# Performance work log

Hardware: AMD Instinct MI355X
Metric: run time of the kernel (lower is better)

## Reference

```python
import jax, jax.numpy as jnp
import numpy as np
import math

N_HEAD = 16
ROPE_BASE = 10000.0


def _rope_cos_sin(seq_len, head_dim, dtype):
    # standard RoPE tables: freqs_i = base^(-2i/d), i in [0, d/2)
    half = head_dim // 2
    inv_freq = ROPE_BASE ** (-(jnp.arange(half, dtype=jnp.float32) * 2.0 / head_dim))
    t = jnp.arange(seq_len, dtype=jnp.float32)
    ang = t[:, None] * inv_freq[None, :]  # [S, d/2]
    return jnp.cos(ang).astype(dtype), jnp.sin(ang).astype(dtype)


def _apply_rope(x, cos, sin):
    # x: [B, S, H, d]; rotate interleaved even/odd pairs
    x1 = x[..., 0::2]
    x2 = x[..., 1::2]
    c = cos[None, :, None, :]
    s = sin[None, :, None, :]
    out = jnp.stack([x1 * c - x2 * s, x1 * s + x2 * c], axis=-1)
    return out.reshape(x.shape)


def setup_inputs() -> dict:
    key = jax.random.key(0)
    kx, kq, kk, kv, ko = jax.random.split(key, 5)
    B, S, H = 2, 2048, 1024
    x = jax.random.normal(kx, (B, S, H), dtype=jnp.float32)
    scale = 0.02
    w_q = jax.random.normal(kq, (H, H), dtype=jnp.float32) * scale
    w_k = jax.random.normal(kk, (H, H), dtype=jnp.float32) * scale
    w_v = jax.random.normal(kv, (H, H), dtype=jnp.float32) * scale
    w_o = jax.random.normal(ko, (H, H), dtype=jnp.float32) * scale
    return {"x": x, "w_q": w_q, "w_k": w_k, "w_v": w_v, "w_o": w_o}


def reference(x, w_q, w_k, w_v, w_o):
    B, S, H = x.shape
    d = H // N_HEAD
    # torch nn.Linear(bias=False): y = x @ W^T, W is [out, in]
    q = (x @ w_q.T).reshape(B, S, N_HEAD, d)
    k = (x @ w_k.T).reshape(B, S, N_HEAD, d)
    v = (x @ w_v.T).reshape(B, S, N_HEAD, d)
    cos, sin = _rope_cos_sin(S, d, x.dtype)
    q = _apply_rope(q, cos, sin)
    k = _apply_rope(k, cos, sin)
    scores = jnp.einsum("bqhd,bkhd->bhqk", q, k) / math.sqrt(d)
    coefs = jax.nn.softmax(scores, axis=-1)
    # NOTE: causal mask is applied AFTER softmax via tril (no renormalization)
    causal = jnp.tril(jnp.ones((S, S), dtype=bool))
    coefs = jnp.where(causal[None, None], coefs, 0.0)
    out = jnp.einsum("bhqk,bkhd->bqhd", coefs, v).reshape(B, S, H)
    return out @ w_o.T
```

## Files before the change

kernel.cpp:

```cpp
#include <hip/hip_runtime.h>
#include <math.h>

#define SEQ   2048
#define HDIM  1024
#define NH    16
#define DH    64
#define MTOT  4096
#define BHTOT 32

typedef _Float16 half_t;
typedef __attribute__((ext_vector_type(2))) __fp16 fp16x2;
typedef __attribute__((ext_vector_type(4))) _Float16 half4;
typedef __attribute__((ext_vector_type(8))) _Float16 half8;
typedef __attribute__((ext_vector_type(4))) float float4v;

typedef __attribute__((address_space(1))) const unsigned int guint;
typedef __attribute__((address_space(3))) unsigned int luint;
__device__ __forceinline__ void glds16(const half_t* g, half_t* l) {
    __builtin_amdgcn_global_load_lds((guint*)g, (luint*)l, 16, 0, 0);
}

__global__ __launch_bounds__(256)
void prep(const float* __restrict__ x,  const float* __restrict__ wq,
          const float* __restrict__ wk, const float* __restrict__ wv,
          const float* __restrict__ wo,
          half_t* __restrict__ xh,  half_t* __restrict__ wqh,
          half_t* __restrict__ wkh, half_t* __restrict__ wvh,
          half_t* __restrict__ woh, float2* __restrict__ rope)
{
    const int bid = blockIdx.x;
    if (bid < 8192) {
        int i = bid * 256 + threadIdx.x;
        const float* s; half_t* d;
        if (i < 1048576) { s = x; d = xh; }
        else {
            int j = i - 1048576;
            int w = j >> 18; i = j & 262143;
            s = (w == 0) ? wq : (w == 1) ? wk : (w == 2) ? wv : wo;
            d = (w == 0) ? wqh : (w == 1) ? wkh : (w == 2) ? wvh : woh;
        }
        float4 v = ((const float4*)s)[i];
        union { half_t h[4]; uint2 u; } tmp;
        tmp.h[0] = (half_t)v.x; tmp.h[1] = (half_t)v.y;
        tmp.h[2] = (half_t)v.z; tmp.h[3] = (half_t)v.w;
        ((uint2*)d)[i] = tmp.u;
    } else {
        int tt = (bid - 8192) * 256 + threadIdx.x;
        int s = tt >> 5, j = tt & 31;
        float inv = powf(10000.0f, -(float)j / 32.0f);
        float ang = (float)s * inv;
        rope[tt] = make_float2(cosf(ang), sinf(ang));
    }
}

__global__ __launch_bounds__(256)
void gemm_qkv(const half_t* __restrict__ A,
              const half_t* __restrict__ w0, const half_t* __restrict__ w1,
              const half_t* __restrict__ w2,
              half_t* __restrict__ Qb, half_t* __restrict__ Kb,
              half_t* __restrict__ Vtb,
              const float2* __restrict__ rope)
{
    const int mode = blockIdx.z;
    const half_t* Bw = (mode == 1) ? w1 : (mode == 2) ? w2 : w0;

    __shared__ __align__(16) half_t Ash[128][32];
    __shared__ __align__(16) half_t Bsh[128][32];
    __shared__ __align__(16) half_t Esh[4][32][72];

    const int t    = threadIdx.x;
    const int lane = t & 63;
    const int wave = t >> 6;
    const int quad = lane >> 4;
    const int l16  = lane & 15;
    const int wr   = (wave >> 1) * 64;
    const int wc   = (wave & 1) * 64;
    const int bm   = blockIdx.x, bn = blockIdx.y;

    const int srow = lane >> 2, spos = lane & 3;
    const half_t* Asrc0 = A  + (size_t)(bm * 128 + wave * 32      + srow) * HDIM + spos * 8;
    const half_t* Asrc1 = A  + (size_t)(bm * 128 + wave * 32 + 16 + srow) * HDIM + spos * 8;
    const half_t* Bsrc0 = Bw + (size_t)(bn * 128 + wave * 32      + srow) * HDIM + spos * 8;
    const half_t* Bsrc1 = Bw + (size_t)(bn * 128 + wave * 32 + 16 + srow) * HDIM + spos * 8;
    half_t* Adst0 = &Ash[wave * 32][0];
    half_t* Adst1 = &Ash[wave * 32 + 16][0];
    half_t* Bdst0 = &Bsh[wave * 32][0];
    half_t* Bdst1 = &Bsh[wave * 32 + 16][0];

    float4v acc[4][4] = {};

    for (int kt = 0; kt < HDIM / 32; ++kt) {
        glds16(Asrc0, Adst0);
        glds16(Asrc1, Adst1);
        glds16(Bsrc0, Bdst0);
        glds16(Bsrc1, Bdst1);
        Asrc0 += 32; Asrc1 += 32; Bsrc0 += 32; Bsrc1 += 32;
        __syncthreads();
        half8 af[4], bf[4];
#pragma unroll
        for (int mb = 0; mb < 4; ++mb) af[mb] = *(const half8*)&Ash[wr + mb * 16 + l16][quad * 8];
#pragma unroll
        for (int nb = 0; nb < 4; ++nb) bf[nb] = *(const half8*)&Bsh[wc + nb * 16 + l16][quad * 8];
#pragma unroll
        for (int mb = 0; mb < 4; ++mb)
#pragma unroll
            for (int nb = 0; nb < 4; ++nb)
                acc[mb][nb] = __builtin_amdgcn_mfma_f32_16x16x32_f16(af[mb], bf[nb], acc[mb][nb], 0, 0, 0);
        __syncthreads();
    }

    if (mode == 2) {
#pragma unroll
        for (int mb = 0; mb < 4; ++mb)
#pragma unroll
            for (int nb = 0; nb < 4; ++nb) {
                int row0 = bm * 128 + wr + mb * 16 + quad * 4;
                int col  = bn * 128 + wc + nb * 16 + l16;
                int b = row0 >> 11, s0 = row0 & 2047;
                int h = col >> 6,  dd = col & 63;
                union { half_t h4[4]; uint2 u; } tmp;
#pragma unroll
                for (int r = 0; r < 4; ++r) tmp.h4[r] = (half_t)acc[mb][nb][r];
                *(uint2*)&Vtb[((size_t)((b * NH + h) * DH + dd)) * SEQ + s0] = tmp.u;
            }
        return;
    }
    {
        half_t* Ob = (mode == 0) ? Qb : Kb;
        const float scl = (mode == 0) ? 0.125f * 1.44269504088896f : 1.0f;
        const int h = (bn * 128 + wc) >> 6;
#pragma unroll
        for (int mh = 0; mh < 2; ++mh) {
#pragma unroll
            for (int mb2 = 0; mb2 < 2; ++mb2) {
                const int mb = mh * 2 + mb2;
                const int row0 = bm * 128 + wr + mb * 16 + quad * 4;
#pragma unroll
                for (int nb = 0; nb < 4; ++nb) {
                    const int dd = nb * 16 + l16;
                    const int jj = dd >> 1;
#pragma unroll
                    for (int r = 0; r < 4; ++r) {
                        float v  = acc[mb][nb][r];
                        float vp = __shfl_xor(v, 1, 64);
                        int s = (row0 + r) & 2047;
                        float2 cs = rope[s * 32 + jj];
                        float res = ((dd & 1) == 0) ? (v * cs.x - vp * cs.y)
                                                    : (vp * cs.y + v * cs.x);
                        Esh[wave][mb2 * 16 + quad * 4 + r][dd] = (half_t)(res * scl);
                    }
                }
            }
            __asm__ volatile("s_waitcnt lgkmcnt(0)" ::: "memory");
#pragma unroll
            for (int c = 0; c < 4; ++c) {
                int uidx = c * 64 + lane;
                int row = uidx >> 3, ch = uidx & 7;
                uint4 v = *(const uint4*)&Esh[wave][row][ch * 8];
                int sg = bm * 128 + wr + mh * 32 + row;
                int b = sg >> 11, s = sg & 2047;
                *(uint4*)&Ob[((size_t)((b * NH + h) * SEQ + s)) * DH + ch * 8] = v;
            }
        }
    }
}

__global__ __launch_bounds__(256)
void gemm_out(const half_t* __restrict__ A, const half_t* __restrict__ W,
              float* __restrict__ outF)
{
    __shared__ __align__(16) half_t Ash[64][32];
    __shared__ __align__(16) half_t Bsh[128][32];

    const int t    = threadIdx.x;
    const int lane = t & 63;
    const int wave = t >> 6;
    const int quad = lane >> 4;
    const int l16  = lane & 15;
    const int wr   = (wave >> 1) * 32;
    const int wc   = (wave & 1) * 64;
    const int bm   = blockIdx.x, bn = blockIdx.y;

    const int srow = lane >> 2, spos = lane & 3;
    const half_t* Asrc  = A + (size_t)(bm * 64 + wave * 16 + srow) * HDIM + spos * 8;
    half_t* Adst = &Ash[wave * 16][0];
    const half_t* Bsrc0 = W + (size_t)(bn * 128 + wave * 32      + srow) * HDIM + spos * 8;
    const half_t* Bsrc1 = W + (size_t)(bn * 128 + wave * 32 + 16 + srow) * HDIM + spos * 8;
    half_t* Bdst0 = &Bsh[wave * 32][0];
    half_t* Bdst1 = &Bsh[wave * 32 + 16][0];

    float4v acc[2][4] = {};

    for (int kt = 0; kt < HDIM / 32; ++kt) {
        glds16(Asrc, Adst);
        glds16(Bsrc0, Bdst0);
        glds16(Bsrc1, Bdst1);
        Asrc += 32; Bsrc0 += 32; Bsrc1 += 32;
        __syncthreads();
        half8 af[2], bf[4];
#pragma unroll
        for (int mb = 0; mb < 2; ++mb) af[mb] = *(const half8*)&Ash[wr + mb * 16 + l16][quad * 8];
#pragma unroll
        for (int nb = 0; nb < 4; ++nb) bf[nb] = *(const half8*)&Bsh[wc + nb * 16 + l16][quad * 8];
#pragma unroll
        for (int mb = 0; mb < 2; ++mb)
#pragma unroll
            for (int nb = 0; nb < 4; ++nb)
                acc[mb][nb] = __builtin_amdgcn_mfma_f32_16x16x32_f16(af[mb], bf[nb], acc[mb][nb], 0, 0, 0);
        __syncthreads();
    }

#pragma unroll
    for (int mb = 0; mb < 2; ++mb)
#pragma unroll
        for (int nb = 0; nb < 4; ++nb) {
            int row0 = bm * 64 + wr + mb * 16 + quad * 4;
            int col  = bn * 128 + wc + nb * 16 + l16;
#pragma unroll
            for (int r = 0; r < 4; ++r)
                outF[(size_t)(row0 + r) * HDIM + col] = acc[mb][nb][r];
        }
}

__global__ __launch_bounds__(512)
void attn_fused(const half_t* __restrict__ Qb, const half_t* __restrict__ Kb,
                const half_t* __restrict__ Vtb, half_t* __restrict__ AOut)
{
    const int jb = blockIdx.x;
    const int bh = blockIdx.y;

    __shared__ __align__(16) half_t Ksh[2][64][64];
    __shared__ __align__(16) half_t Vsh[2][64][72];

    const int t = threadIdx.x;
    const int wave = t >> 6, lane = t & 63, quad = lane >> 4, l16 = lane & 15;
    const int unit = wave >> 2, wl = wave & 3;
    const int qtile = unit ? (15 - jb) : jb;
    const int q0 = qtile * 128 + wl * 32;
    const int ktop = 2 * (15 - jb) + 1;

    half8 qf[2][2];
#pragma unroll
    for (int g = 0; g < 2; ++g) {
        const half_t* Qp = Qb + ((size_t)bh * SEQ + q0 + g * 16 + l16) * DH + quad * 8;
        qf[g][0] = *(const half8*)Qp;
        qf[g][1] = *(const half8*)(Qp + 32);
    }

    float4v o[2][4] = {};
    float lsum[2] = {0.f, 0.f};

    const int krow = lane >> 3, kpos = lane & 7;
    const int kchunk = kpos ^ krow;
    const half_t* Ksrc0 = Kb + ((size_t)bh * SEQ + wl * 16     + krow) * DH + kchunk * 8;
    const half_t* Ksrc1 = Kb + ((size_t)bh * SEQ + wl * 16 + 8 + krow) * DH + kchunk * 8;
    const int ko1 = ((quad ^ (l16 & 7)) * 8);
    const int ko2 = ko1 ^ 32;

    const int tv  = t & 255;
    const int sr  = tv >> 2;
    const int scc = (tv & 3) * 16;
    const half_t* Vg = Vtb + ((size_t)bh * DH + sr) * SEQ + scc;

    if (unit == 0) {
        glds16(Ksrc0, &Ksh[0][wl * 16][0]);
        glds16(Ksrc1, &Ksh[0][wl * 16 + 8][0]);
    } else {
        *(uint4*)&Vsh[0][sr][scc]     = *(const uint4*)(Vg);
        *(uint4*)&Vsh[0][sr][scc + 8] = *(const uint4*)(Vg + 8);
    }
    __syncthreads();

    for (int kt = 0; kt < SEQ / 64; ++kt) {
        const int cur = kt & 1, nxt = cur ^ 1;
        const bool have_next = (kt + 1 < SEQ / 64);
        const bool next_v    = (kt + 1 <= ktop);

        uint4 va, vb;
        if (unit == 0) {
            if (have_next) {
                const half_t* Kn = Ksrc0 + (size_t)(kt + 1) * 64 * DH;
                glds16(Kn,          &Ksh[nxt][wl * 16][0]);
                glds16(Kn + 8 * DH, &Ksh[nxt][wl * 16 + 8][0]);
            }
        } else if (have_next && next_v) {
            const half_t* Vgk = Vg + (kt + 1) * 64;
            va = *(const uint4*)(Vgk);
            vb = *(const uint4*)(Vgk + 8);
        }

        float4v sc[2][4];
#pragma unroll
        for (int nb = 0; nb < 4; ++nb) {
            const half_t* kp = &Ksh[cur][nb * 16 + l16][0];
            half8 kf0 = *(const half8*)(kp + ko1);
            half8 kf1 = *(const half8*)(kp + ko2);
#pragma unroll
            for (int g = 0; g < 2; ++g) {
                float4v a = {};
                a = __builtin_amdgcn_mfma_f32_16x16x32_f16(kf0, qf[g][0], a, 0, 0, 0);
                a = __builtin_amdgcn_mfma_f32_16x16x32_f16(kf1, qf[g][1], a, 0, 0, 0);
                sc[g][nb] = a;
            }
        }

#pragma unroll
        for (int g = 0; g < 2; ++g)
#pragma unroll
            for (int nb = 0; nb < 4; ++nb)
#pragma unroll
                for (int r = 0; r < 4; ++r) {
                    float e = __builtin_amdgcn_exp2f(sc[g][nb][r]);
                    sc[g][nb][r] = e;
                    lsum[g] += e;
                }

        const int kbase = kt * 64;
        if (kbase <= q0 + 31) {
            if (kbase + 63 > q0) {
#pragma unroll
                for (int g = 0; g < 2; ++g) {
                    int qg = q0 + g * 16 + l16;
#pragma unroll
                    for (int nb = 0; nb < 4; ++nb)
#pragma unroll
                        for (int r = 0; r < 4; ++r)
                            if (kbase + nb * 16 + quad * 4 + r > qg) sc[g][nb][r] = 0.f;
                }
            }
            half4 pf[2][4];
#pragma unroll
            for (int g = 0; g < 2; ++g)
#pragma unroll
                for (int nb = 0; nb < 4; ++nb) {
                    union { fp16x2 v2[2]; half4 v4; } u;
                    u.v2[0] = __builtin_amdgcn_cvt_pkrtz(sc[g][nb][0], sc[g][nb][1]);
                    u.v2[1] = __builtin_amdgcn_cvt_pkrtz(sc[g][nb][2], sc[g][nb][3]);
                    pf[g][nb] = u.v4;
                }
#pragma unroll
            for (int md = 0; md < 4; ++md)
#pragma unroll
                for (int nb = 0; nb < 4; ++nb) {
                    half4 vf = *(const half4*)&Vsh[cur][md * 16 + l16][nb * 16 + quad * 4];
                    o[0][md] = __builtin_amdgcn_mfma_f32_16x16x16f16(vf, pf[0][nb], o[0][md], 0, 0, 0);
                    o[1][md] = __builtin_amdgcn_mfma_f32_16x16x16f16(vf, pf[1][nb], o[1][md], 0, 0, 0);
                }
        }

        if (unit == 1 && have_next && next_v) {
            *(uint4*)&Vsh[nxt][sr][scc]     = va;
            *(uint4*)&Vsh[nxt][sr][scc + 8] = vb;
        }
        __syncthreads();
    }

    const int b = bh >> 4, h = bh & 15;
    const int orow = lane >> 2, occ = (lane & 3) * 16;
    half_t* scr = unit ? ((half_t*)Vsh + wl * 1152) : ((half_t*)Ksh + wl * 1152);
    half_t (*Osh)[72] = (half_t(*)[72])scr;
#pragma unroll
    for (int g = 0; g < 2; ++g) {
        float rs = lsum[g];
        rs += __shfl_xor(rs, 16, 64);
        rs += __shfl_xor(rs, 32, 64);
        const float inv = 1.0f / rs;
#pragma unroll
        for (int md = 0; md < 4; ++md)
#pragma unroll
            for (int r = 0; r < 4; ++r)
                Osh[l16][md * 16 + quad * 4 + r] = (half_t)(o[g][md][r] * inv);
        __asm__ volatile("s_waitcnt lgkmcnt(0)" ::: "memory");
        uint4 o0 = *(const uint4*)&Osh[orow][occ];
        uint4 o1 = *(const uint4*)&Osh[orow][occ + 8];
        const int s = q0 + g * 16 + orow;
        half_t* dst = AOut + ((size_t)(b * SEQ + s)) * HDIM + h * DH + occ;
        *(uint4*)dst       = o0;
        *(uint4*)(dst + 8) = o1;
    }
}

extern "C" void kernel_launch(void* const* d_in, const int* in_sizes, int n_in,
                              void* d_out, int out_size, void* d_ws, size_t ws_size,
                              hipStream_t stream)
{
    const float* x  = (const float*)d_in[0];
    const float* wq = (const float*)d_in[1];
    const float* wk = (const float*)d_in[2];
    const float* wv = (const float*)d_in[3];
    const float* wo = (const float*)d_in[4];
    float* out = (float*)d_out;

    char* ws = (char*)d_ws;
    size_t off = 0;
    auto alloc = [&](size_t bytes) -> void* {
        void* p = ws + off;
        off += (bytes + 255) & ~(size_t)255;
        return p;
    };
    half_t* xh   = (half_t*)alloc((size_t)MTOT * HDIM * 2);
    half_t* wqh  = (half_t*)alloc((size_t)HDIM * HDIM * 2);
    half_t* wkh  = (half_t*)alloc((size_t)HDIM * HDIM * 2);
    half_t* wvh  = (half_t*)alloc((size_t)HDIM * HDIM * 2);
    half_t* woh  = (half_t*)alloc((size_t)HDIM * HDIM * 2);
    half_t* Qb   = (half_t*)alloc((size_t)BHTOT * SEQ * DH * 2);
    half_t* Kb   = (half_t*)alloc((size_t)BHTOT * SEQ * DH * 2);
    half_t* Vtb  = (half_t*)alloc((size_t)BHTOT * SEQ * DH * 2);
    half_t* ah   = (half_t*)alloc((size_t)MTOT * HDIM * 2);
    float2* rope = (float2*)alloc((size_t)SEQ * 32 * sizeof(float2));

    prep<<<8448, 256, 0, stream>>>(x, wq, wk, wv, wo, xh, wqh, wkh, wvh, woh, rope);

    gemm_qkv<<<dim3(32, 8, 3), 256, 0, stream>>>(xh, wqh, wkh, wvh,
                                                 Qb, Kb, Vtb, rope);
    attn_fused<<<dim3(8, 32), 512, 0, stream>>>(Qb, Kb, Vtb, ah);
    gemm_out<<<dim3(64, 8), 256, 0, stream>>>(ah, woh, out);
}
```

Baseline: 193.3 us.

## Widen GEMM K-tile to 64 with XOR-swizzled LDS, restructure RoPE epilogue, add setprio

```diff
diff --git a/kernel.cpp b/kernel.cpp
--- a/kernel.cpp
+++ b/kernel.cpp
@@ -64,9 +64,9 @@
     const int mode = blockIdx.z;
     const half_t* Bw = (mode == 1) ? w1 : (mode == 2) ? w2 : w0;
 
-    __shared__ __align__(16) half_t Ash[128][32];
-    __shared__ __align__(16) half_t Bsh[128][32];
-    __shared__ __align__(16) half_t Esh[4][32][72];
+    __shared__ __align__(16) half_t Tsh[2][128][64];
+    half_t (*Ash)[64] = Tsh[0];
+    half_t (*Bsh)[64] = Tsh[1];
 
     const int t    = threadIdx.x;
     const int lane = t & 63;
@@ -77,35 +77,40 @@
     const int wc   = (wave & 1) * 64;
     const int bm   = blockIdx.x, bn = blockIdx.y;
 
-    const int srow = lane >> 2, spos = lane & 3;
-    const half_t* Asrc0 = A  + (size_t)(bm * 128 + wave * 32      + srow) * HDIM + spos * 8;
-    const half_t* Asrc1 = A  + (size_t)(bm * 128 + wave * 32 + 16 + srow) * HDIM + spos * 8;
-    const half_t* Bsrc0 = Bw + (size_t)(bn * 128 + wave * 32      + srow) * HDIM + spos * 8;
-    const half_t* Bsrc1 = Bw + (size_t)(bn * 128 + wave * 32 + 16 + srow) * HDIM + spos * 8;
-    half_t* Adst0 = &Ash[wave * 32][0];
-    half_t* Adst1 = &Ash[wave * 32 + 16][0];
-    half_t* Bdst0 = &Bsh[wave * 32][0];
-    half_t* Bdst1 = &Bsh[wave * 32 + 16][0];
+    const int srow   = lane >> 3;
+    const int schunk = (lane & 7) ^ srow;
+    const half_t* Asrc = A  + (size_t)(bm * 128 + srow) * HDIM + schunk * 8;
+    const half_t* Bsrc = Bw + (size_t)(bn * 128 + srow) * HDIM + schunk * 8;
+    const int swz = (l16 & 7) << 4;
 
     float4v acc[4][4] = {};
 
-    for (int kt = 0; kt < HDIM / 32; ++kt) {
-        glds16(Asrc0, Adst0);
-        glds16(Asrc1, Adst1);
-        glds16(Bsrc0, Bdst0);
-        glds16(Bsrc1, Bdst1);
-        Asrc0 += 32; Asrc1 += 32; Bsrc0 += 32; Bsrc1 += 32;
+    for (int kt = 0; kt < HDIM / 64; ++kt) {
+        const half_t* Ak = Asrc + kt * 64;
+        const half_t* Bk = Bsrc + kt * 64;
+#pragma unroll
+        for (int c = 0; c < 4; ++c) {
+            const int r8 = wave * 32 + c * 8;
+            glds16(Ak + (size_t)r8 * HDIM, &Ash[r8][0]);
+            glds16(Bk + (size_t)r8 * HDIM, &Bsh[r8][0]);
+        }
         __syncthreads();
-        half8 af[4], bf[4];
-#pragma unroll
-        for (int mb = 0; mb < 4; ++mb) af[mb] = *(const half8*)&Ash[wr + mb * 16 + l16][quad * 8];
-#pragma unroll
-        for (int nb = 0; nb < 4; ++nb) bf[nb] = *(const half8*)&Bsh[wc + nb * 16 + l16][quad * 8];
-#pragma unroll
-        for (int mb = 0; mb < 4; ++mb)
+#pragma unroll
+        for (int kk = 0; kk < 2; ++kk) {
+            const int cb = ((quad << 4) | (kk << 6)) ^ swz;
+            half8 af[4], bf[4];
+#pragma unroll
+            for (int mb = 0; mb < 4; ++mb)
+                af[mb] = *(const half8*)((const char*)&Ash[wr + mb * 16 + l16][0] + cb);
 #pragma unroll
             for (int nb = 0; nb < 4; ++nb)
-                acc[mb][nb] = __builtin_amdgcn_mfma_f32_16x16x32_f16(af[mb], bf[nb], acc[mb][nb], 0, 0, 0);
+                bf[nb] = *(const half8*)((const char*)&Bsh[wc + nb * 16 + l16][0] + cb);
+#pragma unroll
+            for (int mb = 0; mb < 4; ++mb)
+#pragma unroll
+                for (int nb = 0; nb < 4; ++nb)
+                    acc[mb][nb] = __builtin_amdgcn_mfma_f32_16x16x32_f16(af[mb], bf[nb], acc[mb][nb], 0, 0, 0);
+        }
         __syncthreads();
     }
 
@@ -129,37 +134,37 @@
         half_t* Ob = (mode == 0) ? Qb : Kb;
         const float scl = (mode == 0) ? 0.125f * 1.44269504088896f : 1.0f;
         const int h = (bn * 128 + wc) >> 6;
-#pragma unroll
-        for (int mh = 0; mh < 2; ++mh) {
-#pragma unroll
-            for (int mb2 = 0; mb2 < 2; ++mb2) {
-                const int mb = mh * 2 + mb2;
-                const int row0 = bm * 128 + wr + mb * 16 + quad * 4;
-#pragma unroll
-                for (int nb = 0; nb < 4; ++nb) {
-                    const int dd = nb * 16 + l16;
-                    const int jj = dd >> 1;
-#pragma unroll
-                    for (int r = 0; r < 4; ++r) {
-                        float v  = acc[mb][nb][r];
-                        float vp = __shfl_xor(v, 1, 64);
-                        int s = (row0 + r) & 2047;
-                        float2 cs = rope[s * 32 + jj];
-                        float res = ((dd & 1) == 0) ? (v * cs.x - vp * cs.y)
-                                                    : (vp * cs.y + v * cs.x);
-                        Esh[wave][mb2 * 16 + quad * 4 + r][dd] = (half_t)(res * scl);
-                    }
-                }
-            }
+        float* E = (float*)&Tsh[0][0][0] + wave * 1088;
+#pragma unroll
+        for (int mb = 0; mb < 4; ++mb) {
+#pragma unroll
+            for (int nb = 0; nb < 4; ++nb)
+#pragma unroll
+                for (int r = 0; r < 4; ++r)
+                    E[(quad * 4 + r) * 68 + nb * 16 + l16] = acc[mb][nb][r];
             __asm__ volatile("s_waitcnt lgkmcnt(0)" ::: "memory");
 #pragma unroll
-            for (int c = 0; c < 4; ++c) {
-                int uidx = c * 64 + lane;
-                int row = uidx >> 3, ch = uidx & 7;
-                uint4 v = *(const uint4*)&Esh[wave][row][ch * 8];
-                int sg = bm * 128 + wr + mh * 32 + row;
-                int b = sg >> 11, s = sg & 2047;
-                *(uint4*)&Ob[((size_t)((b * NH + h) * SEQ + s)) * DH + ch * 8] = v;
+            for (int c = 0; c < 2; ++c) {
+                const int uidx = c * 64 + lane;
+                const int row = uidx >> 3, ch = uidx & 7;
+                const int sg = bm * 128 + wr + mb * 16 + row;
+                const int b = sg >> 11, s = sg & 2047;
+                const float* Er = E + row * 68 + ch * 8;
+                const float4 e0 = *(const float4*)Er;
+                const float4 e1 = *(const float4*)(Er + 4);
+                const float4* rp = (const float4*)(rope + (size_t)s * 32 + ch * 4);
+                const float4 r01 = rp[0];
+                const float4 r23 = rp[1];
+                union { half_t hh[8]; uint4 u; } o;
+                o.hh[0] = (half_t)((e0.x * r01.x - e0.y * r01.y) * scl);
+                o.hh[1] = (half_t)((e0.x * r01.y + e0.y * r01.x) * scl);
+                o.hh[2] = (half_t)((e0.z * r01.z - e0.w * r01.w) * scl);
+                o.hh[3] = (half_t)((e0.z * r01.w + e0.w * r01.z) * scl);
+                o.hh[4] = (half_t)((e1.x * r23.x - e1.y * r23.y) * scl);
+                o.hh[5] = (half_t)((e1.x * r23.y + e1.y * r23.x) * scl);
+                o.hh[6] = (half_t)((e1.z * r23.z - e1.w * r23.w) * scl);
+                o.hh[7] = (half_t)((e1.z * r23.w + e1.w * r23.z) * scl);
+                *(uint4*)&Ob[((size_t)((b * NH + h) * SEQ + s)) * DH + ch * 8] = o.u;
             }
         }
     }
@@ -169,8 +174,8 @@
 void gemm_out(const half_t* __restrict__ A, const half_t* __restrict__ W,
               float* __restrict__ outF)
 {
-    __shared__ __align__(16) half_t Ash[64][32];
-    __shared__ __align__(16) half_t Bsh[128][32];
+    __shared__ __align__(16) half_t Ash[64][64];
+    __shared__ __align__(16) half_t Bsh[128][64];
 
     const int t    = threadIdx.x;
     const int lane = t & 63;
@@ -181,32 +186,44 @@
     const int wc   = (wave & 1) * 64;
     const int bm   = blockIdx.x, bn = blockIdx.y;
 
-    const int srow = lane >> 2, spos = lane & 3;
-    const half_t* Asrc  = A + (size_t)(bm * 64 + wave * 16 + srow) * HDIM + spos * 8;
-    half_t* Adst = &Ash[wave * 16][0];
-    const half_t* Bsrc0 = W + (size_t)(bn * 128 + wave * 32      + srow) * HDIM + spos * 8;
-    const half_t* Bsrc1 = W + (size_t)(bn * 128 + wave * 32 + 16 + srow) * HDIM + spos * 8;
-    half_t* Bdst0 = &Bsh[wave * 32][0];
-    half_t* Bdst1 = &Bsh[wave * 32 + 16][0];
+    const int srow   = lane >> 3;
+    const int schunk = (lane & 7) ^ srow;
+    const half_t* Asrc = A + (size_t)(bm * 64  + srow) * HDIM + schunk * 8;
+    const half_t* Bsrc = W + (size_t)(bn * 128 + srow) * HDIM + schunk * 8;
+    const int swz = (l16 & 7) << 4;
 
     float4v acc[2][4] = {};
 
-    for (int kt = 0; kt < HDIM / 32; ++kt) {
-        glds16(Asrc, Adst);
-        glds16(Bsrc0, Bdst0);
-        glds16(Bsrc1, Bdst1);
-        Asrc += 32; Bsrc0 += 32; Bsrc1 += 32;
+    for (int kt = 0; kt < HDIM / 64; ++kt) {
+        const half_t* Ak = Asrc + kt * 64;
+        const half_t* Bk = Bsrc + kt * 64;
+#pragma unroll
+        for (int c = 0; c < 2; ++c) {
+            const int r8 = wave * 16 + c * 8;
+            glds16(Ak + (size_t)r8 * HDIM, &Ash[r8][0]);
+        }
+#pragma unroll
+        for (int c = 0; c < 4; ++c) {
+            const int r8 = wave * 32 + c * 8;
+            glds16(Bk + (size_t)r8 * HDIM, &Bsh[r8][0]);
+        }
         __syncthreads();
-        half8 af[2], bf[4];
-#pragma unroll
-        for (int mb = 0; mb < 2; ++mb) af[mb] = *(const half8*)&Ash[wr + mb * 16 + l16][quad * 8];
-#pragma unroll
-        for (int nb = 0; nb < 4; ++nb) bf[nb] = *(const half8*)&Bsh[wc + nb * 16 + l16][quad * 8];
-#pragma unroll
-        for (int mb = 0; mb < 2; ++mb)
+#pragma unroll
+        for (int kk = 0; kk < 2; ++kk) {
+            const int cb = ((quad << 4) | (kk << 6)) ^ swz;
+            half8 af[2], bf[4];
+#pragma unroll
+            for (int mb = 0; mb < 2; ++mb)
+                af[mb] = *(const half8*)((const char*)&Ash[wr + mb * 16 + l16][0] + cb);
 #pragma unroll
             for (int nb = 0; nb < 4; ++nb)
-                acc[mb][nb] = __builtin_amdgcn_mfma_f32_16x16x32_f16(af[mb], bf[nb], acc[mb][nb], 0, 0, 0);
+                bf[nb] = *(const half8*)((const char*)&Bsh[wc + nb * 16 + l16][0] + cb);
+#pragma unroll
+            for (int mb = 0; mb < 2; ++mb)
+#pragma unroll
+                for (int nb = 0; nb < 4; ++nb)
+                    acc[mb][nb] = __builtin_amdgcn_mfma_f32_16x16x32_f16(af[mb], bf[nb], acc[mb][nb], 0, 0, 0);
+        }
         __syncthreads();
     }
 
@@ -290,6 +307,7 @@
         }
 
         float4v sc[2][4];
+        __builtin_amdgcn_s_setprio(1);
 #pragma unroll
         for (int nb = 0; nb < 4; ++nb) {
             const half_t* kp = &Ksh[cur][nb * 16 + l16][0];
@@ -303,6 +321,7 @@
                 sc[g][nb] = a;
             }
         }
+        __builtin_amdgcn_s_setprio(0);
 
 #pragma unroll
         for (int g = 0; g < 2; ++g)
@@ -338,6 +357,7 @@
                     u.v2[1] = __builtin_amdgcn_cvt_pkrtz(sc[g][nb][2], sc[g][nb][3]);
                     pf[g][nb] = u.v4;
                 }
+            __builtin_amdgcn_s_setprio(1);
 #pragma unroll
             for (int md = 0; md < 4; ++md)
 #pragma unroll
@@ -346,6 +366,7 @@
                     o[0][md] = __builtin_amdgcn_mfma_f32_16x16x16f16(vf, pf[0][nb], o[0][md], 0, 0, 0);
                     o[1][md] = __builtin_amdgcn_mfma_f32_16x16x16f16(vf, pf[1][nb], o[1][md], 0, 0, 0);
                 }
+            __builtin_amdgcn_s_setprio(0);
         }
 
         if (unit == 1 && have_next && next_v) {
```

After: 190.2 us. About the same (-1.6%).
